# Kernel optimization log

Measured on AMD Instinct MI355X. Metric: run time of the kernel, lower is better.

The kernel has to match this reference:

```python
import jax, jax.numpy as jnp
import numpy as np

N = 50000
E = 600000


def setup_inputs() -> dict:
    key = jax.random.key(0)
    ks = jax.random.split(key, 8)
    x = jax.random.normal(ks[0], (N, 128), dtype=jnp.float32)
    # guarantee every node appears at least once as a source (row) so deg > 0
    row_extra = jax.random.randint(ks[1], (E - N,), 0, N, dtype=jnp.int32)
    row = jnp.concatenate([jnp.arange(N, dtype=jnp.int32), row_extra])
    col = jax.random.randint(ks[2], (E,), 0, N, dtype=jnp.int32)
    edge_index = jnp.stack([row, col])  # [2, E]
    edge_weight = jax.random.uniform(ks[3], (E,), dtype=jnp.float32, minval=0.1, maxval=1.0)
    s1 = 1.0 / np.sqrt(128)
    W1 = jax.random.normal(ks[4], (128, 128), dtype=jnp.float32) * s1
    b1 = jnp.zeros((128,), dtype=jnp.float32)
    W2 = jax.random.normal(ks[5], (128, 128), dtype=jnp.float32) * s1
    b2 = jnp.zeros((128,), dtype=jnp.float32)
    return {"x": x, "edge_index": edge_index, "edge_weight": edge_weight,
            "W1": W1, "b1": b1, "W2": W2, "b2": b2}


def _gcn_layer(x, row, col, edge_weight, W, b):
    # dense linear (torch Linear: x @ W.T + b)
    h = x @ W.T + b  # [N, d_out]
    n = h.shape[0]
    # degree via scatter-add of edge weights over source nodes
    deg = jax.ops.segment_sum(edge_weight, row, num_segments=n)  # [N]
    deg_inv_sqrt = deg ** -0.5
    norm = deg_inv_sqrt[row] * edge_weight * deg_inv_sqrt[col]  # [E]
    # message: gather source features, scale, scatter-add to targets
    msg = norm[:, None] * h[row]  # [E, d_out]
    return jax.ops.segment_sum(msg, col, num_segments=n)  # [N, d_out]


def reference(x, edge_index, edge_weight, W1, b1, W2, b2):
    row, col = edge_index[0], edge_index[1]
    h = _gcn_layer(x, row, col, edge_weight, W1, b1)
    h = jax.nn.relu(h)
    return _gcn_layer(h, row, col, edge_weight, W2, b2)
```

## Files before the change

### kernel.cpp

```cpp
#include <hip/hip_runtime.h>

#define DF 128
#define CAP 40

__global__ void build_kernel(const int* __restrict__ row, const int* __restrict__ col,
                             const float* __restrict__ w,
                             float* __restrict__ deg, int* __restrict__ cnt,
                             int2* __restrict__ csr, int E) {
    int e = blockIdx.x * blockDim.x + threadIdx.x;
    if (e < E) {
        int r = row[e], c = col[e];
        float wv = w[e];
        atomicAdd(&deg[r], wv);
        int pos = atomicAdd(&cnt[c], 1);
        if (pos < CAP)
            csr[(size_t)c * CAP + pos] = make_int2(r, __float_as_int(wv));
    }
}

__global__ void dis_kernel(const float* __restrict__ deg, float* __restrict__ dis, int N) {
    int n = blockIdx.x * blockDim.x + threadIdx.x;
    if (n < N) dis[n] = rsqrtf(deg[n]);
}

#define TROWS 64
__global__ __launch_bounds__(256) void gemm_kernel(
    const float* __restrict__ X, const float* __restrict__ W,
    const float* __restrict__ b, float* __restrict__ H, int nrows)
{
    __shared__ float Xs[TROWS * DF];
    __shared__ float Wsk[32 * DF];

    const int tid  = threadIdx.x;
    const int rgrp = tid >> 5;
    const int cgrp = tid & 31;
    const int n0   = blockIdx.x * TROWS;

#pragma unroll
    for (int i = 0; i < 8; ++i) {
        int idx = tid + i * 256;
        int r   = idx >> 5;
        int kk  = idx & 31;
        int n   = n0 + r;
        float4 v = make_float4(0.f, 0.f, 0.f, 0.f);
        if (n < nrows) v = ((const float4*)(X + (size_t)n * DF))[kk];
        ((float4*)Xs)[idx] = v;
    }

    float4 acc[8];
    const float4 bias = ((const float4*)b)[cgrp];
#pragma unroll
    for (int r = 0; r < 8; ++r) acc[r] = bias;

    const float4* Xs4 = (const float4*)Xs;
    const float4* Ws4 = (const float4*)Wsk;

    for (int k0 = 0; k0 < DF; k0 += 32) {
        __syncthreads();
#pragma unroll
        for (int i = 0; i < 4; ++i) {
            int idx = tid + i * 256;
            int c   = idx >> 3;
            int kk  = idx & 7;
            float4 v = ((const float4*)(W + (size_t)c * DF + k0))[kk];
            int kb = kk * 4;
            Wsk[(kb + 0) * DF + c] = v.x;
            Wsk[(kb + 1) * DF + c] = v.y;
            Wsk[(kb + 2) * DF + c] = v.z;
            Wsk[(kb + 3) * DF + c] = v.w;
        }
        __syncthreads();

#pragma unroll
        for (int kk = 0; kk < 8; ++kk) {
            const int kb = (k0 >> 2) + kk;
            float4 w0 = Ws4[(kk * 4 + 0) * 32 + cgrp];
            float4 w1 = Ws4[(kk * 4 + 1) * 32 + cgrp];
            float4 w2 = Ws4[(kk * 4 + 2) * 32 + cgrp];
            float4 w3 = Ws4[(kk * 4 + 3) * 32 + cgrp];
#pragma unroll
            for (int r = 0; r < 8; ++r) {
                float4 x4 = Xs4[(rgrp * 8 + r) * 32 + kb];
                acc[r].x = fmaf(x4.x, w0.x, acc[r].x);
                acc[r].y = fmaf(x4.x, w0.y, acc[r].y);
                acc[r].z = fmaf(x4.x, w0.z, acc[r].z);
                acc[r].w = fmaf(x4.x, w0.w, acc[r].w);
                acc[r].x = fmaf(x4.y, w1.x, acc[r].x);
                acc[r].y = fmaf(x4.y, w1.y, acc[r].y);
                acc[r].z = fmaf(x4.y, w1.z, acc[r].z);
                acc[r].w = fmaf(x4.y, w1.w, acc[r].w);
                acc[r].x = fmaf(x4.z, w2.x, acc[r].x);
                acc[r].y = fmaf(x4.z, w2.y, acc[r].y);
                acc[r].z = fmaf(x4.z, w2.z, acc[r].z);
                acc[r].w = fmaf(x4.z, w2.w, acc[r].w);
                acc[r].x = fmaf(x4.w, w3.x, acc[r].x);
                acc[r].y = fmaf(x4.w, w3.y, acc[r].y);
                acc[r].z = fmaf(x4.w, w3.z, acc[r].z);
                acc[r].w = fmaf(x4.w, w3.w, acc[r].w);
            }
        }
    }

#pragma unroll
    for (int r = 0; r < 8; ++r) {
        int n = n0 + rgrp * 8 + r;
        if (n < nrows) ((float4*)(H + (size_t)n * DF))[cgrp] = acc[r];
    }
}

template <bool RELU_OUT>
__global__ void agg_kernel(const float4* __restrict__ H4,
                           const int2* __restrict__ csr, const int* __restrict__ cnt,
                           const float* __restrict__ dis,
                           float4* __restrict__ O4, int N)
{
    const int gid  = blockIdx.x * blockDim.x + threadIdx.x;
    const int node = gid >> 5;
    const int t    = gid & 31;
    if (node >= N) return;
    int m = cnt[node];
    if (m > CAP) m = CAP;
    const int2* bucket = csr + (size_t)node * CAP;
    const float dcol = dis[node];
    float4 acc = make_float4(0.f, 0.f, 0.f, 0.f);
    for (int i = 0; i < m; ++i) {
        const int2 rec = bucket[i];
        const int   s  = rec.x;
        const float wv = __int_as_float(rec.y) * dis[s];
        float4 h = H4[(size_t)s * 32 + t];
        acc.x = fmaf(wv, h.x, acc.x);
        acc.y = fmaf(wv, h.y, acc.y);
        acc.z = fmaf(wv, h.z, acc.z);
        acc.w = fmaf(wv, h.w, acc.w);
    }
    acc.x *= dcol; acc.y *= dcol; acc.z *= dcol; acc.w *= dcol;
    if (RELU_OUT) {
        acc.x = fmaxf(acc.x, 0.f); acc.y = fmaxf(acc.y, 0.f);
        acc.z = fmaxf(acc.z, 0.f); acc.w = fmaxf(acc.w, 0.f);
    }
    O4[(size_t)node * 32 + t] = acc;
}

extern "C" void kernel_launch(void* const* d_in, const int* in_sizes, int n_in,
                              void* d_out, int out_size, void* d_ws, size_t ws_size,
                              hipStream_t stream) {
    const float* x  = (const float*)d_in[0];
    const int*   ei = (const int*)d_in[1];
    const float* ew = (const float*)d_in[2];
    const float* W1 = (const float*)d_in[3];
    const float* b1 = (const float*)d_in[4];
    const float* W2 = (const float*)d_in[5];
    const float* b2 = (const float*)d_in[6];
    float* out = (float*)d_out;

    const int E = in_sizes[2];
    const int N = in_sizes[0] / DF;
    const int* row = ei;
    const int* col = ei + E;

    char* ws = (char*)d_ws;
    size_t offb = 0;
    auto alloc = [&](size_t bytes) { char* p = ws + offb; offb = (offb + bytes + 511) & ~(size_t)511; return p; };
    float* deg  = (float*)alloc((size_t)2 * N * 4);
    int*   cnt  = (int*)(deg + N);
    float* dis  = (float*)alloc((size_t)N * 4);
    int2*  csr  = (int2*)alloc((size_t)N * CAP * 8);
    float* h1   = (float*)alloc((size_t)N * DF * 4);
    float* agg1 = (float*)alloc((size_t)N * DF * 4);
    (void)ws_size;

    hipMemsetAsync(deg, 0, (size_t)2 * N * 4, stream);

    const int TB = 256;
    const int eblocks = (E + TB - 1) / TB;

    build_kernel<<<eblocks, TB, 0, stream>>>(row, col, ew, deg, cnt, csr, E);
    dis_kernel<<<(N + TB - 1) / TB, TB, 0, stream>>>(deg, dis, N);

    const int gemm_blocks = (N + TROWS - 1) / TROWS;
    gemm_kernel<<<gemm_blocks, 256, 0, stream>>>(x, W1, b1, h1, N);
    const int agg_blocks = (N * 32 + TB - 1) / TB;
    agg_kernel<true><<<agg_blocks, TB, 0, stream>>>((const float4*)h1, csr, cnt, dis,
                                                    (float4*)agg1, N);
    gemm_kernel<<<gemm_blocks, 256, 0, stream>>>(agg1, W2, b2, h1, N);
    agg_kernel<false><<<agg_blocks, TB, 0, stream>>>((const float4*)h1, csr, cnt, dis,
                                                     (float4*)out, N);
}
```

Measured before the change: 320.6 us.

## Fuse graph build into first GEMM launch and compute rsqrt inline in aggregation

```diff
diff --git a/kernel.cpp b/kernel.cpp
--- a/kernel.cpp
+++ b/kernel.cpp
@@ -2,36 +2,34 @@
 
 #define DF 128
 #define CAP 40
-
-__global__ void build_kernel(const int* __restrict__ row, const int* __restrict__ col,
-                             const float* __restrict__ w,
-                             float* __restrict__ deg, int* __restrict__ cnt,
-                             int2* __restrict__ csr, int E) {
-    int e = blockIdx.x * blockDim.x + threadIdx.x;
-    if (e < E) {
-        int r = row[e], c = col[e];
-        float wv = w[e];
-        atomicAdd(&deg[r], wv);
-        int pos = atomicAdd(&cnt[c], 1);
-        if (pos < CAP)
-            csr[(size_t)c * CAP + pos] = make_int2(r, __float_as_int(wv));
-    }
-}
-
-__global__ void dis_kernel(const float* __restrict__ deg, float* __restrict__ dis, int N) {
-    int n = blockIdx.x * blockDim.x + threadIdx.x;
-    if (n < N) dis[n] = rsqrtf(deg[n]);
-}
-
 #define TROWS 64
-__global__ __launch_bounds__(256) void gemm_kernel(
+
+__global__ __launch_bounds__(256) void build_gemm_kernel(
     const float* __restrict__ X, const float* __restrict__ W,
-    const float* __restrict__ b, float* __restrict__ H, int nrows)
+    const float* __restrict__ b, float* __restrict__ H, int nrows,
+    const int* __restrict__ row, const int* __restrict__ col,
+    const float* __restrict__ ew,
+    float* __restrict__ deg, int* __restrict__ cnt, int2* __restrict__ csr,
+    int E, int gemmBlocks)
 {
     __shared__ float Xs[TROWS * DF];
     __shared__ float Wsk[32 * DF];
 
-    const int tid  = threadIdx.x;
+    const int tid = threadIdx.x;
+
+    if (blockIdx.x >= gemmBlocks) {
+        int e = (blockIdx.x - gemmBlocks) * 256 + tid;
+        if (e < E) {
+            int r = row[e], c = col[e];
+            float wv = ew[e];
+            atomicAdd(&deg[r], wv);
+            int pos = atomicAdd(&cnt[c], 1);
+            if (pos < CAP)
+                csr[(size_t)c * CAP + pos] = make_int2(r, __float_as_int(wv));
+        }
+        return;
+    }
+
     const int rgrp = tid >> 5;
     const int cgrp = tid & 31;
     const int n0   = blockIdx.x * TROWS;
@@ -108,10 +106,94 @@
     }
 }
 
+__global__ __launch_bounds__(256) void gemm_kernel(
+    const float* __restrict__ X, const float* __restrict__ W,
+    const float* __restrict__ b, float* __restrict__ H, int nrows)
+{
+    __shared__ float Xs[TROWS * DF];
+    __shared__ float Wsk[32 * DF];
+
+    const int tid  = threadIdx.x;
+    const int rgrp = tid >> 5;
+    const int cgrp = tid & 31;
+    const int n0   = blockIdx.x * TROWS;
+
+#pragma unroll
+    for (int i = 0; i < 8; ++i) {
+        int idx = tid + i * 256;
+        int r   = idx >> 5;
+        int kk  = idx & 31;
+        int n   = n0 + r;
+        float4 v = make_float4(0.f, 0.f, 0.f, 0.f);
+        if (n < nrows) v = ((const float4*)(X + (size_t)n * DF))[kk];
+        ((float4*)Xs)[idx] = v;
+    }
+
+    float4 acc[8];
+    const float4 bias = ((const float4*)b)[cgrp];
+#pragma unroll
+    for (int r = 0; r < 8; ++r) acc[r] = bias;
+
+    const float4* Xs4 = (const float4*)Xs;
+    const float4* Ws4 = (const float4*)Wsk;
+
+    for (int k0 = 0; k0 < DF; k0 += 32) {
+        __syncthreads();
+#pragma unroll
+        for (int i = 0; i < 4; ++i) {
+            int idx = tid + i * 256;
+            int c   = idx >> 3;
+            int kk  = idx & 7;
+            float4 v = ((const float4*)(W + (size_t)c * DF + k0))[kk];
+            int kb = kk * 4;
+            Wsk[(kb + 0) * DF + c] = v.x;
+            Wsk[(kb + 1) * DF + c] = v.y;
+            Wsk[(kb + 2) * DF + c] = v.z;
+            Wsk[(kb + 3) * DF + c] = v.w;
+        }
+        __syncthreads();
+
+#pragma unroll
+        for (int kk = 0; kk < 8; ++kk) {
+            const int kb = (k0 >> 2) + kk;
+            float4 w0 = Ws4[(kk * 4 + 0) * 32 + cgrp];
+            float4 w1 = Ws4[(kk * 4 + 1) * 32 + cgrp];
+            float4 w2 = Ws4[(kk * 4 + 2) * 32 + cgrp];
+            float4 w3 = Ws4[(kk * 4 + 3) * 32 + cgrp];
+#pragma unroll
+            for (int r = 0; r < 8; ++r) {
+                float4 x4 = Xs4[(rgrp * 8 + r) * 32 + kb];
+                acc[r].x = fmaf(x4.x, w0.x, acc[r].x);
+                acc[r].y = fmaf(x4.x, w0.y, acc[r].y);
+                acc[r].z = fmaf(x4.x, w0.z, acc[r].z);
+                acc[r].w = fmaf(x4.x, w0.w, acc[r].w);
+                acc[r].x = fmaf(x4.y, w1.x, acc[r].x);
+                acc[r].y = fmaf(x4.y, w1.y, acc[r].y);
+                acc[r].z = fmaf(x4.y, w1.z, acc[r].z);
+                acc[r].w = fmaf(x4.y, w1.w, acc[r].w);
+                acc[r].x = fmaf(x4.z, w2.x, acc[r].x);
+                acc[r].y = fmaf(x4.z, w2.y, acc[r].y);
+                acc[r].z = fmaf(x4.z, w2.z, acc[r].z);
+                acc[r].w = fmaf(x4.z, w2.w, acc[r].w);
+                acc[r].x = fmaf(x4.w, w3.x, acc[r].x);
+                acc[r].y = fmaf(x4.w, w3.y, acc[r].y);
+                acc[r].z = fmaf(x4.w, w3.z, acc[r].z);
+                acc[r].w = fmaf(x4.w, w3.w, acc[r].w);
+            }
+        }
+    }
+
+#pragma unroll
+    for (int r = 0; r < 8; ++r) {
+        int n = n0 + rgrp * 8 + r;
+        if (n < nrows) ((float4*)(H + (size_t)n * DF))[cgrp] = acc[r];
+    }
+}
+
 template <bool RELU_OUT>
 __global__ void agg_kernel(const float4* __restrict__ H4,
                            const int2* __restrict__ csr, const int* __restrict__ cnt,
-                           const float* __restrict__ dis,
+                           const float* __restrict__ deg,
                            float4* __restrict__ O4, int N)
 {
     const int gid  = blockIdx.x * blockDim.x + threadIdx.x;
@@ -121,12 +203,12 @@
     int m = cnt[node];
     if (m > CAP) m = CAP;
     const int2* bucket = csr + (size_t)node * CAP;
-    const float dcol = dis[node];
+    const float dcol = rsqrtf(deg[node]);
     float4 acc = make_float4(0.f, 0.f, 0.f, 0.f);
     for (int i = 0; i < m; ++i) {
         const int2 rec = bucket[i];
         const int   s  = rec.x;
-        const float wv = __int_as_float(rec.y) * dis[s];
+        const float wv = __int_as_float(rec.y) * rsqrtf(deg[s]);
         float4 h = H4[(size_t)s * 32 + t];
         acc.x = fmaf(wv, h.x, acc.x);
         acc.y = fmaf(wv, h.y, acc.y);
@@ -163,7 +245,6 @@
     auto alloc = [&](size_t bytes) { char* p = ws + offb; offb = (offb + bytes + 511) & ~(size_t)511; return p; };
     float* deg  = (float*)alloc((size_t)2 * N * 4);
     int*   cnt  = (int*)(deg + N);
-    float* dis  = (float*)alloc((size_t)N * 4);
     int2*  csr  = (int2*)alloc((size_t)N * CAP * 8);
     float* h1   = (float*)alloc((size_t)N * DF * 4);
     float* agg1 = (float*)alloc((size_t)N * DF * 4);
@@ -173,16 +254,15 @@
 
     const int TB = 256;
     const int eblocks = (E + TB - 1) / TB;
-
-    build_kernel<<<eblocks, TB, 0, stream>>>(row, col, ew, deg, cnt, csr, E);
-    dis_kernel<<<(N + TB - 1) / TB, TB, 0, stream>>>(deg, dis, N);
-
     const int gemm_blocks = (N + TROWS - 1) / TROWS;
-    gemm_kernel<<<gemm_blocks, 256, 0, stream>>>(x, W1, b1, h1, N);
+
+    build_gemm_kernel<<<gemm_blocks + eblocks, 256, 0, stream>>>(
+        x, W1, b1, h1, N, row, col, ew, deg, cnt, csr, E, gemm_blocks);
+
     const int agg_blocks = (N * 32 + TB - 1) / TB;
-    agg_kernel<true><<<agg_blocks, TB, 0, stream>>>((const float4*)h1, csr, cnt, dis,
+    agg_kernel<true><<<agg_blocks, TB, 0, stream>>>((const float4*)h1, csr, cnt, deg,
                                                     (float4*)agg1, N);
     gemm_kernel<<<gemm_blocks, 256, 0, stream>>>(agg1, W2, b2, h1, N);
-    agg_kernel<false><<<agg_blocks, TB, 0, stream>>>((const float4*)h1, csr, cnt, dis,
+    agg_kernel<false><<<agg_blocks, TB, 0, stream>>>((const float4*)h1, csr, cnt, deg,
                                                      (float4*)out, N);
 }
```

Result: faster. 299.1 us (-6.7%).
